# Kernel optimization log

Measured on AMD Instinct MI355X. Metric: run time of the kernel, lower is better.

The kernel has to match this reference:

```python
import jax, jax.numpy as jnp
import numpy as np

B, LQ, LK, D, H, DK = 128, 32, 128, 1024, 16, 64


def setup_inputs() -> dict:
    key = jax.random.key(0)
    ks = jax.random.split(key, 10)
    Q_seq = jax.random.normal(ks[0], (B, LQ, D), dtype=jnp.float32)
    K_seq = jax.random.normal(ks[1], (B, LK, D), dtype=jnp.float32)
    V_seq = jax.random.normal(ks[2], (B, LK, D), dtype=jnp.float32)
    title_mask = (jax.random.uniform(ks[3], (B, LQ)) < 0.9).astype(jnp.float32)
    body_mask = (jax.random.uniform(ks[4], (B, LQ, LK)) < 0.9).astype(jnp.float32)
    s = 1.0 / np.sqrt(D)
    Wq = jax.random.uniform(ks[5], (H * DK, D), jnp.float32, -s, s)
    Wk = jax.random.uniform(ks[6], (H * DK, D), jnp.float32, -s, s)
    Wv = jax.random.uniform(ks[7], (H * DK, D), jnp.float32, -s, s)
    bq = jnp.zeros((H * DK,), jnp.float32)
    bk = jnp.zeros((H * DK,), jnp.float32)
    bv = jnp.zeros((H * DK,), jnp.float32)
    return {"Q_seq": Q_seq, "K_seq": K_seq, "V_seq": V_seq,
            "title_mask": title_mask, "body_mask": body_mask,
            "Wq": Wq, "bq": bq, "Wk": Wk, "bk": bk, "Wv": Wv, "bv": bv}


def reference(Q_seq, K_seq, V_seq, title_mask, body_mask, Wq, bq, Wk, bk, Wv, bv):
    b = Q_seq.shape[0]
    # concatenate title tokens onto keys/values: [B, LK+LQ, D]
    K_cat = jnp.concatenate([K_seq, Q_seq], axis=1)
    V_cat = jnp.concatenate([V_seq, Q_seq], axis=1)
    # mask: [B, LQ, LK+LQ]
    tmask_rep = jnp.broadcast_to(title_mask[:, None, :], (b, LQ, LQ))
    mask = jnp.concatenate([body_mask, tmask_rep], axis=2) * title_mask[:, :, None]
    # projections -> [B, H, len, DK]
    Qh = (Q_seq @ Wq.T + bq).reshape(b, LQ, H, DK).transpose(0, 2, 1, 3)
    Kh = (K_cat @ Wk.T + bk).reshape(b, LK + LQ, H, DK).transpose(0, 2, 1, 3)
    Vh = (V_cat @ Wv.T + bv).reshape(b, LK + LQ, H, DK).transpose(0, 2, 1, 3)
    # custom exp-based masked attention (non-softmax normalization)
    scores = jnp.einsum('bhqd,bhkd->bhqk', Qh, Kh) / np.sqrt(float(DK))
    scores = jnp.exp(scores) * mask[:, None, :, :]
    attn = scores / (jnp.sum(scores, axis=-1, keepdims=True) + 1e-8)
    ctx = jnp.einsum('bhqk,bhkd->bhqd', attn, Vh)
    return ctx.transpose(0, 2, 1, 3).reshape(b, LQ, H * DK)
```

## Files before the change

### kernel.cpp

```cpp
#include <hip/hip_runtime.h>

typedef _Float16 f16;
typedef _Float16 f16x2 __attribute__((ext_vector_type(2)));
typedef _Float16 f16x4 __attribute__((ext_vector_type(4)));
typedef _Float16 f16x8 __attribute__((ext_vector_type(8)));
typedef float f32x4v __attribute__((ext_vector_type(4)));

#define AS1 __attribute__((address_space(1)))
#define AS3 __attribute__((address_space(3)))

__device__ __forceinline__ void gload_lds16(const f16* g, f16* l) {
  __builtin_amdgcn_global_load_lds((const AS1 unsigned int*)g,
                                   (AS3 unsigned int*)l, 16, 0, 0);
}

__global__ __launch_bounds__(256) void prep_kernel(
    const float* __restrict__ Q_seq, const float* __restrict__ K_seq,
    const float* __restrict__ V_seq,
    const float* __restrict__ Wq, const float* __restrict__ Wk,
    const float* __restrict__ Wv,
    f16* __restrict__ Qb, f16* __restrict__ Kb, f16* __restrict__ Vb,
    f16* __restrict__ Wqb, f16* __restrict__ Wkb, f16* __restrict__ Wvb)
{
  const long long g = (long long)blockIdx.x * 256 + threadIdx.x;
  const float* s;
  f16* d;
  if (g < 524288) {
    s = Q_seq + g * 8; d = Qb + g * 8;
  } else if (g < 2621440) {
    long long e = (g - 524288) * 8; s = K_seq + e; d = Kb + e;
  } else if (g < 4718592) {
    long long e = (g - 2621440) * 8; s = V_seq + e; d = Vb + e;
  } else if (g < 4849664) {
    long long e = (g - 4718592) * 8; s = Wq + e; d = Wqb + e;
  } else if (g < 4980736) {
    long long e = (g - 4849664) * 8; s = Wk + e; d = Wkb + e;
  } else {
    long long e = (g - 4980736) * 8; s = Wv + e; d = Wvb + e;
  }
  float4 v0 = *(const float4*)s;
  float4 v1 = *(const float4*)(s + 4);
  f16x8 o;
  o[0] = (f16)v0.x; o[1] = (f16)v0.y; o[2] = (f16)v0.z; o[3] = (f16)v0.w;
  o[4] = (f16)v1.x; o[5] = (f16)v1.y; o[6] = (f16)v1.z; o[7] = (f16)v1.w;
  *(f16x8*)d = o;
}

__device__ __forceinline__ void gemm_tile_256(
    const f16* __restrict__ A, const f16* __restrict__ W,
    const float* __restrict__ bias, f16* __restrict__ C,
    int m0, int n0, int rowShift, int outStride, int rowOff,
    f16* sbuf)
{
  const int t = threadIdx.x;
  const int w = t >> 6, lane = t & 63;
  const int wr = w >> 2, wc = w & 3;
  const int fr = lane & 15, g = lane >> 4;
  const int lrow = lane >> 3;
  const int kgr = (lane & 7) ^ lrow;

  const f16* aSrc[4];
  const f16* bSrc[4];
#pragma unroll
  for (int s = 0; s < 4; ++s) {
    aSrc[s] = A + (long long)(m0 + (w * 4 + s) * 8 + lrow) * 1024 + kgr * 8;
    bSrc[s] = W + (long long)(n0 + (w * 4 + s) * 8 + lrow) * 1024 + kgr * 8;
  }

#define STAGE(tile)                                                          \
  {                                                                          \
    f16* ab_ = sbuf + (((tile) & 1) << 15);                                  \
    const int ko_ = (tile) * 64;                                             \
    _Pragma("unroll") for (int s = 0; s < 4; ++s)                            \
        gload_lds16(aSrc[s] + ko_, ab_ + (w * 4 + s) * 512);                 \
    _Pragma("unroll") for (int s = 0; s < 4; ++s)                            \
        gload_lds16(bSrc[s] + ko_, ab_ + 16384 + (w * 4 + s) * 512);         \
  }

  const int gk0 = ((0 + g) ^ (fr & 7)) * 8;
  const int gk1 = ((4 + g) ^ (fr & 7)) * 8;
  const int aoff = (wr * 128 + fr) * 64;
  const int boff = (wc * 64 + fr) * 64;

  f32x4v acc[8][4];
#pragma unroll
  for (int i = 0; i < 8; ++i)
#pragma unroll
    for (int j = 0; j < 4; ++j) acc[i][j] = (f32x4v){0.f, 0.f, 0.f, 0.f};

  STAGE(0);
  STAGE(1);

  for (int tt = 0; tt < 16; ++tt) {
    if (tt < 15) {
      asm volatile("s_waitcnt vmcnt(8)" ::: "memory");
    } else {
      asm volatile("s_waitcnt vmcnt(0)" ::: "memory");
    }
    __builtin_amdgcn_s_barrier();
    __builtin_amdgcn_sched_barrier(0);

    const f16* ab = sbuf + ((tt & 1) << 15);
    const f16* bb = ab + 16384;

    f16x8 av0[8], bv0[4], av1[8], bv1[4];
#pragma unroll
    for (int i = 0; i < 8; ++i)
      av0[i] = *(const f16x8*)(ab + aoff + i * 1024 + gk0);
#pragma unroll
    for (int j = 0; j < 4; ++j)
      bv0[j] = *(const f16x8*)(bb + boff + j * 1024 + gk0);
    __builtin_amdgcn_sched_barrier(0);
#pragma unroll
    for (int i = 0; i < 8; ++i)
      av1[i] = *(const f16x8*)(ab + aoff + i * 1024 + gk1);
#pragma unroll
    for (int j = 0; j < 4; ++j)
      bv1[j] = *(const f16x8*)(bb + boff + j * 1024 + gk1);

    asm volatile("s_waitcnt lgkmcnt(12)" ::: "memory");
    __builtin_amdgcn_sched_barrier(0);
    __builtin_amdgcn_s_setprio(1);
#pragma unroll
    for (int i = 0; i < 8; ++i)
#pragma unroll
      for (int j = 0; j < 4; ++j)
        acc[i][j] = __builtin_amdgcn_mfma_f32_16x16x32_f16(av0[i], bv0[j],
                                                           acc[i][j], 0, 0, 0);
    __builtin_amdgcn_s_setprio(0);

    asm volatile("s_waitcnt lgkmcnt(0)" ::: "memory");
    __builtin_amdgcn_sched_barrier(0);
    __builtin_amdgcn_s_barrier();
    __builtin_amdgcn_sched_barrier(0);
    if (tt < 14) STAGE(tt + 2);
    __builtin_amdgcn_sched_barrier(0);
    __builtin_amdgcn_s_setprio(1);
#pragma unroll
    for (int i = 0; i < 8; ++i)
#pragma unroll
      for (int j = 0; j < 4; ++j)
        acc[i][j] = __builtin_amdgcn_mfma_f32_16x16x32_f16(av1[i], bv1[j],
                                                           acc[i][j], 0, 0, 0);
    __builtin_amdgcn_s_setprio(0);
  }
#undef STAGE

  f16* Cs = sbuf;
  float bn[4];
#pragma unroll
  for (int j = 0; j < 4; ++j) bn[j] = bias[n0 + wc * 64 + j * 16 + fr];
#pragma unroll
  for (int i = 0; i < 8; ++i) {
#pragma unroll
    for (int j = 0; j < 4; ++j) {
#pragma unroll
      for (int v = 0; v < 4; ++v) {
        int row = wr * 128 + i * 16 + g * 4 + v;
        int col = wc * 64 + j * 16 + fr;
        Cs[row * 256 + (col ^ (((row >> 2) & 7) << 3))] =
            (f16)(acc[i][j][v] + bn[j]);
      }
    }
  }
  __syncthreads();

  const int rowMask = (1 << rowShift) - 1;
  const int row = t >> 1, half = t & 1;
  const int csw = ((row >> 2) & 7) << 3;
  const int arow = m0 + row;
  const int orow = (arow >> rowShift) * outStride + (arow & rowMask) + rowOff;
  f16* dst = C + (long long)orow * 1024 + n0 + half * 128;
  const f16* srcr = Cs + row * 256;
#pragma unroll
  for (int c = 0; c < 16; ++c)
    *(f16x8*)(dst + c * 8) = *(const f16x8*)(srcr + ((half * 128 + c * 8) ^ csw));
}

__global__ __launch_bounds__(512, 1) void gemm_all(
    const f16* __restrict__ Qb, const f16* __restrict__ Kb,
    const f16* __restrict__ Vb,
    const f16* __restrict__ Wqb, const f16* __restrict__ Wkb,
    const f16* __restrict__ Wvb,
    const float* __restrict__ bq, const float* __restrict__ bk,
    const float* __restrict__ bv,
    f16* __restrict__ Qh, f16* __restrict__ Kh, f16* __restrict__ Vh)
{
  __shared__ __align__(16) f16 sbuf[65536];
  const int bid = blockIdx.x;
  const int v = (bid & 7) * 88 + (bid >> 3);

  const f16* A;
  const f16* W;
  const float* bias;
  f16* C;
  int m0, n0, rowShift, outStride, rowOff;

  if (v < 512) {
    const int z = v >> 8, rem = v & 255;
    A = z ? Vb : Kb;
    W = z ? Wvb : Wkb;
    bias = z ? bv : bk;
    C = z ? Vh : Kh;
    m0 = (rem >> 2) * 256; n0 = (rem & 3) * 256;
    rowShift = 7; outStride = 160; rowOff = 0;
  } else {
    const int u = v - 512;
    const int z = u >> 6, rem = u & 63;
    A = Qb;
    W = (z == 0) ? Wqb : (z == 1) ? Wkb : Wvb;
    bias = (z == 0) ? bq : (z == 1) ? bk : bv;
    C = (z == 0) ? Qh : (z == 1) ? Kh : Vh;
    m0 = (rem >> 2) * 256; n0 = (rem & 3) * 256;
    rowShift = 5;
    outStride = (z == 0) ? 32 : 160;
    rowOff = (z == 0) ? 0 : 128;
  }
  gemm_tile_256(A, W, bias, C, m0, n0, rowShift, outStride, rowOff, sbuf);
}

__global__ __launch_bounds__(256) void attn_kernel(
    const f16* __restrict__ Qh, const f16* __restrict__ Kh,
    const f16* __restrict__ Vh,
    const float* __restrict__ title, const float* __restrict__ body,
    float* __restrict__ out)
{
  __shared__ __align__(16) f16 Qs[32 * 72];
  __shared__ __align__(16) f16 Ks[160 * 72];
  __shared__ __align__(16) f16 Vs[160 * 68];
  __shared__ float rs[4][32];
  __shared__ float invs[32];

  const int bh = blockIdx.x, b = bh >> 4, h = bh & 15;
  const int t = threadIdx.x, w = t >> 6, lane = t & 63;
  const int c = lane & 15, g = lane >> 4;

  const long long qbase = ((long long)(b * 32) << 10) + h * 64;
  const long long kbase = ((long long)(b * 160) << 10) + h * 64;

  {
    int row = t >> 3, ch = t & 7;
    *(f16x8*)(Qs + row * 72 + ch * 8) =
        *(const f16x8*)(Qh + qbase + (long long)row * 1024 + ch * 8);
  }
#pragma unroll
  for (int r = 0; r < 5; ++r) {
    int i = t + r * 256;
    int row = i >> 3, ch = i & 7;
    *(f16x8*)(Ks + row * 72 + ch * 8) =
        *(const f16x8*)(Kh + kbase + (long long)row * 1024 + ch * 8);
    f16x8 vv = *(const f16x8*)(Vh + kbase + (long long)row * 1024 + ch * 8);
    f16x4 vlo = __builtin_shufflevector(vv, vv, 0, 1, 2, 3);
    f16x4 vhi = __builtin_shufflevector(vv, vv, 4, 5, 6, 7);
    *(f16x4*)(Vs + row * 68 + ch * 8) = vlo;
    *(f16x4*)(Vs + row * 68 + ch * 8 + 4) = vhi;
  }
  __syncthreads();

  f16x8 qf[2][2];
#pragma unroll
  for (int qt = 0; qt < 2; ++qt)
#pragma unroll
    for (int s = 0; s < 2; ++s)
      qf[qt][s] = *(const f16x8*)(Qs + (qt * 16 + c) * 72 + s * 32 + g * 8);

  const int cnt = (w < 2) ? 3 : 2;
  const int tile0 = (w < 2) ? w * 3 : 6 + (w - 2) * 2;

  f16x4 pp[3][2];
  float rsum[2] = {0.f, 0.f};

#pragma unroll
  for (int i = 0; i < 3; ++i) {
    if (i < cnt) {
      const int kt = tile0 + i;
      f16x8 kf0 = *(const f16x8*)(Ks + (kt * 16 + c) * 72 + 0 + g * 8);
      f16x8 kf1 = *(const f16x8*)(Ks + (kt * 16 + c) * 72 + 32 + g * 8);
#pragma unroll
      for (int qt = 0; qt < 2; ++qt) {
        f32x4v s4 = (f32x4v){0.f, 0.f, 0.f, 0.f};
        s4 = __builtin_amdgcn_mfma_f32_16x16x32_f16(kf0, qf[qt][0], s4, 0, 0, 0);
        s4 = __builtin_amdgcn_mfma_f32_16x16x32_f16(kf1, qf[qt][1], s4, 0, 0, 0);
        float4 m4;
        if (kt < 8) {
          m4 = *(const float4*)(body +
                ((long long)(b * 32 + qt * 16 + c)) * 128 + kt * 16 + 4 * g);
        } else {
          m4 = *(const float4*)(title + b * 32 + (kt - 8) * 16 + 4 * g);
        }
        float e0 = __expf(s4[0] * 0.125f) * m4.x;
        float e1 = __expf(s4[1] * 0.125f) * m4.y;
        float e2 = __expf(s4[2] * 0.125f) * m4.z;
        float e3 = __expf(s4[3] * 0.125f) * m4.w;
        rsum[qt] += (e0 + e1) + (e2 + e3);
        f16x4 p4;
        p4.x = (f16)e0; p4.y = (f16)e1; p4.z = (f16)e2; p4.w = (f16)e3;
        pp[i][qt] = p4;
      }
    }
  }

#pragma unroll
  for (int qt = 0; qt < 2; ++qt) {
    rsum[qt] += __shfl_xor(rsum[qt], 16);
    rsum[qt] += __shfl_xor(rsum[qt], 32);
  }
  if (lane < 16) {
    rs[w][c] = rsum[0];
    rs[w][16 + c] = rsum[1];
  }
  __syncthreads();

  f16* Ps = Ks;
#pragma unroll
  for (int i = 0; i < 3; ++i) {
    if (i < cnt) {
      const int kt = tile0 + i;
#pragma unroll
      for (int qt = 0; qt < 2; ++qt)
        *(f16x4*)(Ps + (qt * 16 + c) * 168 + kt * 16 + 4 * g) = pp[i][qt];
    }
  }
  if (t < 32) {
    float ssum = rs[0][t] + rs[1][t] + rs[2][t] + rs[3][t];
    invs[t] = title[b * 32 + t] / (ssum + 1e-8f);
  }
  __syncthreads();

  f32x4v o[2] = {(f32x4v){0.f, 0.f, 0.f, 0.f}, (f32x4v){0.f, 0.f, 0.f, 0.f}};
#pragma unroll
  for (int s = 0; s < 5; ++s) {
    f16x8 vf;
#pragma unroll
    for (int j = 0; j < 8; ++j)
      vf[j] = Vs[(32 * s + 8 * g + j) * 68 + 16 * w + c];
#pragma unroll
    for (int qt = 0; qt < 2; ++qt) {
      f16x8 pf = *(const f16x8*)(Ps + (qt * 16 + c) * 168 + s * 32 + g * 8);
      o[qt] = __builtin_amdgcn_mfma_f32_16x16x32_f16(pf, vf, o[qt], 0, 0, 0);
    }
  }

#pragma unroll
  for (int qt = 0; qt < 2; ++qt) {
#pragma unroll
    for (int v = 0; v < 4; ++v) {
      int q = qt * 16 + 4 * g + v;
      out[((long long)(b * 32 + q) << 10) + h * 64 + 16 * w + c] =
          o[qt][v] * invs[q];
    }
  }
}

extern "C" void kernel_launch(void* const* d_in, const int* in_sizes, int n_in,
                              void* d_out, int out_size, void* d_ws, size_t ws_size,
                              hipStream_t stream) {
  const float* Q_seq = (const float*)d_in[0];
  const float* K_seq = (const float*)d_in[1];
  const float* V_seq = (const float*)d_in[2];
  const float* title = (const float*)d_in[3];
  const float* body  = (const float*)d_in[4];
  const float* Wq = (const float*)d_in[5];
  const float* bq = (const float*)d_in[6];
  const float* Wk = (const float*)d_in[7];
  const float* bk = (const float*)d_in[8];
  const float* Wv = (const float*)d_in[9];
  const float* bv = (const float*)d_in[10];
  float* out = (float*)d_out;

  f16* ws = (f16*)d_ws;
  f16* Qb  = ws;
  f16* Kb  = Qb + 4194304;
  f16* Vb  = Kb + 16777216;
  f16* Wqb = Vb + 16777216;
  f16* Wkb = Wqb + 1048576;
  f16* Wvb = Wkb + 1048576;
  f16* Qh  = Wvb + 1048576;
  f16* Kh  = Qh + 4194304;
  f16* Vh  = Kh + 20971520;

  prep_kernel<<<19968, 256, 0, stream>>>(Q_seq, K_seq, V_seq, Wq, Wk, Wv,
                                         Qb, Kb, Vb, Wqb, Wkb, Wvb);
  gemm_all<<<704, 512, 0, stream>>>(Qb, Kb, Vb, Wqb, Wkb, Wvb,
                                    bq, bk, bv, Qh, Kh, Vh);
  attn_kernel<<<2048, 256, 0, stream>>>(Qh, Kh, Vh, title, body, out);
}
```

Before: 183.7 us.

## Split GEMM main loop into four barrier-synchronized LDS-read/MFMA phases

Restructures the projection GEMM inner loop from two large phases (read all 12 fragments, then 32 MFMAs) into four smaller phases. Each phase reads half the A fragments plus the B fragments and issues 16 MFMAs, with workgroup barriers between phases. The aim is to cut register pressure (fewer live f16x8 fragments) and to interleave LDS reads with MFMA work across waves in a ping-pong style. In exchange it adds many more s_barrier calls and full lgkmcnt(0) waits per iteration, which could serialize the waves.

```diff
diff --git a/kernel.cpp b/kernel.cpp
--- a/kernel.cpp
+++ b/kernel.cpp
@@ -91,59 +91,70 @@
   STAGE(0);
   STAGE(1);
 
+#define RD_A(dst, ihalf, gk)                                                 \
+  _Pragma("unroll") for (int ii = 0; ii < 4; ++ii)                           \
+      dst[ii] = *(const f16x8*)(ab + aoff + ((ihalf) * 4 + ii) * 1024 + (gk));
+#define RD_B(dst, gk)                                                        \
+  _Pragma("unroll") for (int j = 0; j < 4; ++j)                              \
+      dst[j] = *(const f16x8*)(bb + boff + j * 1024 + (gk));
+#define MFMA16(afr, bfr, ihalf)                                              \
+  __builtin_amdgcn_s_setprio(1);                                             \
+  _Pragma("unroll") for (int ii = 0; ii < 4; ++ii)                           \
+      _Pragma("unroll") for (int j = 0; j < 4; ++j)                          \
+          acc[(ihalf) * 4 + ii][j] = __builtin_amdgcn_mfma_f32_16x16x32_f16( \
+              afr[ii], bfr[j], acc[(ihalf) * 4 + ii][j], 0, 0, 0);           \
+  __builtin_amdgcn_s_setprio(0);
+
   for (int tt = 0; tt < 16; ++tt) {
     if (tt < 15) {
       asm volatile("s_waitcnt vmcnt(8)" ::: "memory");
     } else {
       asm volatile("s_waitcnt vmcnt(0)" ::: "memory");
     }
+    __builtin_amdgcn_sched_barrier(0);
     __builtin_amdgcn_s_barrier();
     __builtin_amdgcn_sched_barrier(0);
 
     const f16* ab = sbuf + ((tt & 1) << 15);
     const f16* bb = ab + 16384;
 
-    f16x8 av0[8], bv0[4], av1[8], bv1[4];
-#pragma unroll
-    for (int i = 0; i < 8; ++i)
-      av0[i] = *(const f16x8*)(ab + aoff + i * 1024 + gk0);
-#pragma unroll
-    for (int j = 0; j < 4; ++j)
-      bv0[j] = *(const f16x8*)(bb + boff + j * 1024 + gk0);
-    __builtin_amdgcn_sched_barrier(0);
-#pragma unroll
-    for (int i = 0; i < 8; ++i)
-      av1[i] = *(const f16x8*)(ab + aoff + i * 1024 + gk1);
-#pragma unroll
-    for (int j = 0; j < 4; ++j)
-      bv1[j] = *(const f16x8*)(bb + boff + j * 1024 + gk1);
-
-    asm volatile("s_waitcnt lgkmcnt(12)" ::: "memory");
-    __builtin_amdgcn_sched_barrier(0);
-    __builtin_amdgcn_s_setprio(1);
-#pragma unroll
-    for (int i = 0; i < 8; ++i)
-#pragma unroll
-      for (int j = 0; j < 4; ++j)
-        acc[i][j] = __builtin_amdgcn_mfma_f32_16x16x32_f16(av0[i], bv0[j],
-                                                           acc[i][j], 0, 0, 0);
-    __builtin_amdgcn_s_setprio(0);
-
+    f16x8 a0[4], a1[4], bf[4];
+
+    RD_A(a0, 0, gk0);
+    RD_B(bf, gk0);
+    __builtin_amdgcn_s_barrier();
     asm volatile("s_waitcnt lgkmcnt(0)" ::: "memory");
     __builtin_amdgcn_sched_barrier(0);
+    MFMA16(a0, bf, 0);
+    __builtin_amdgcn_s_barrier();
+
+    RD_A(a1, 1, gk0);
+    __builtin_amdgcn_s_barrier();
+    asm volatile("s_waitcnt lgkmcnt(0)" ::: "memory");
+    __builtin_amdgcn_sched_barrier(0);
+    MFMA16(a1, bf, 1);
+    __builtin_amdgcn_s_barrier();
+
+    RD_A(a0, 0, gk1);
+    RD_B(bf, gk1);
+    __builtin_amdgcn_s_barrier();
+    asm volatile("s_waitcnt lgkmcnt(0)" ::: "memory");
+    __builtin_amdgcn_sched_barrier(0);
+    MFMA16(a0, bf, 0);
+    __builtin_amdgcn_s_barrier();
+
+    RD_A(a1, 1, gk1);
+    asm volatile("s_waitcnt lgkmcnt(0)" ::: "memory");
+    __builtin_amdgcn_sched_barrier(0);
     __builtin_amdgcn_s_barrier();
     __builtin_amdgcn_sched_barrier(0);
     if (tt < 14) STAGE(tt + 2);
     __builtin_amdgcn_sched_barrier(0);
-    __builtin_amdgcn_s_setprio(1);
-#pragma unroll
-    for (int i = 0; i < 8; ++i)
-#pragma unroll
-      for (int j = 0; j < 4; ++j)
-        acc[i][j] = __builtin_amdgcn_mfma_f32_16x16x32_f16(av1[i], bv1[j],
-                                                           acc[i][j], 0, 0, 0);
-    __builtin_amdgcn_s_setprio(0);
-  }
+    MFMA16(a1, bf, 1);
+  }
+#undef RD_A
+#undef RD_B
+#undef MFMA16
 #undef STAGE
 
   f16* Cs = sbuf;
```

Result: slower. 189.4 us (+3.1%).

## Simplify GEMM main loop to single-stage prefetch with full barriers

Applied to the files above, without the earlier changes.

Replaces the two-deep global-to-LDS prefetch pipeline, which used hand-tuned vmcnt/lgkmcnt waits, split barriers and setprio, with a simpler scheme. Each iteration issues the next tile's loads, computes on the current buffer, and ends with __syncthreads. This removes the manual wait-count bookkeeping and priority toggling, and lets the compiler schedule the LDS reads alongside the MFMAs. In exchange, loads have only one iteration to land, and the full barrier drains all outstanding memory each step, so global latency may be less hidden.

```diff
diff --git a/kernel.cpp b/kernel.cpp
--- a/kernel.cpp
+++ b/kernel.cpp
@@ -89,60 +89,42 @@
     for (int j = 0; j < 4; ++j) acc[i][j] = (f32x4v){0.f, 0.f, 0.f, 0.f};
 
   STAGE(0);
-  STAGE(1);
+  __syncthreads();
 
   for (int tt = 0; tt < 16; ++tt) {
-    if (tt < 15) {
-      asm volatile("s_waitcnt vmcnt(8)" ::: "memory");
-    } else {
-      asm volatile("s_waitcnt vmcnt(0)" ::: "memory");
-    }
-    __builtin_amdgcn_s_barrier();
-    __builtin_amdgcn_sched_barrier(0);
-
     const f16* ab = sbuf + ((tt & 1) << 15);
     const f16* bb = ab + 16384;
 
-    f16x8 av0[8], bv0[4], av1[8], bv1[4];
+    if (tt < 15) STAGE(tt + 1);
+    __builtin_amdgcn_sched_barrier(0);
+
+    f16x8 a0[8], b0[4], a1[8], b1[4];
 #pragma unroll
     for (int i = 0; i < 8; ++i)
-      av0[i] = *(const f16x8*)(ab + aoff + i * 1024 + gk0);
+      a0[i] = *(const f16x8*)(ab + aoff + i * 1024 + gk0);
 #pragma unroll
     for (int j = 0; j < 4; ++j)
-      bv0[j] = *(const f16x8*)(bb + boff + j * 1024 + gk0);
-    __builtin_amdgcn_sched_barrier(0);
+      b0[j] = *(const f16x8*)(bb + boff + j * 1024 + gk0);
 #pragma unroll
     for (int i = 0; i < 8; ++i)
-      av1[i] = *(const f16x8*)(ab + aoff + i * 1024 + gk1);
+#pragma unroll
+      for (int j = 0; j < 4; ++j)
+        acc[i][j] = __builtin_amdgcn_mfma_f32_16x16x32_f16(a0[i], b0[j],
+                                                           acc[i][j], 0, 0, 0);
+#pragma unroll
+    for (int i = 0; i < 8; ++i)
+      a1[i] = *(const f16x8*)(ab + aoff + i * 1024 + gk1);
 #pragma unroll
     for (int j = 0; j < 4; ++j)
-      bv1[j] = *(const f16x8*)(bb + boff + j * 1024 + gk1);
-
-    asm volatile("s_waitcnt lgkmcnt(12)" ::: "memory");
-    __builtin_amdgcn_sched_barrier(0);
-    __builtin_amdgcn_s_setprio(1);
+      b1[j] = *(const f16x8*)(bb + boff + j * 1024 + gk1);
 #pragma unroll
     for (int i = 0; i < 8; ++i)
 #pragma unroll
       for (int j = 0; j < 4; ++j)
-        acc[i][j] = __builtin_amdgcn_mfma_f32_16x16x32_f16(av0[i], bv0[j],
+        acc[i][j] = __builtin_amdgcn_mfma_f32_16x16x32_f16(a1[i], b1[j],
                                                            acc[i][j], 0, 0, 0);
-    __builtin_amdgcn_s_setprio(0);
-
-    asm volatile("s_waitcnt lgkmcnt(0)" ::: "memory");
-    __builtin_amdgcn_sched_barrier(0);
-    __builtin_amdgcn_s_barrier();
-    __builtin_amdgcn_sched_barrier(0);
-    if (tt < 14) STAGE(tt + 2);
-    __builtin_amdgcn_sched_barrier(0);
-    __builtin_amdgcn_s_setprio(1);
-#pragma unroll
-    for (int i = 0; i < 8; ++i)
-#pragma unroll
-      for (int j = 0; j < 4; ++j)
-        acc[i][j] = __builtin_amdgcn_mfma_f32_16x16x32_f16(av1[i], bv1[j],
-                                                           acc[i][j], 0, 0, 0);
-    __builtin_amdgcn_s_setprio(0);
+
+    __syncthreads();
   }
 #undef STAGE
 
```

Result: no change. 182.6 us (-0.6%).

## Interleave per-unit LDS staging with quarter-split MFMA phases in projection GEMM

Applied to the files above, without the earlier changes.

Reworks the projection GEMM main loop. Global-to-LDS copies are split into eight units per tile, and the prefetch of tile tt+1 is spread across four compute sub-phases separated by barriers, instead of staging whole tiles two ahead. A fragments are now loaded per 32-row quarter rather than all at once, which cuts register pressure. The cost is a shorter prefetch distance and more workgroup barriers per k-tile.

```diff
diff --git a/kernel.cpp b/kernel.cpp
--- a/kernel.cpp
+++ b/kernel.cpp
@@ -1,7 +1,6 @@
 #include <hip/hip_runtime.h>
 
 typedef _Float16 f16;
-typedef _Float16 f16x2 __attribute__((ext_vector_type(2)));
 typedef _Float16 f16x4 __attribute__((ext_vector_type(4)));
 typedef _Float16 f16x8 __attribute__((ext_vector_type(8)));
 typedef float f32x4v __attribute__((ext_vector_type(4)));
@@ -56,30 +55,19 @@
   const int w = t >> 6, lane = t & 63;
   const int wr = w >> 2, wc = w & 3;
   const int fr = lane & 15, g = lane >> 4;
-  const int lrow = lane >> 3;
-  const int kgr = (lane & 7) ^ lrow;
-
-  const f16* aSrc[4];
-  const f16* bSrc[4];
-#pragma unroll
-  for (int s = 0; s < 4; ++s) {
-    aSrc[s] = A + (long long)(m0 + (w * 4 + s) * 8 + lrow) * 1024 + kgr * 8;
-    bSrc[s] = W + (long long)(n0 + (w * 4 + s) * 8 + lrow) * 1024 + kgr * 8;
-  }
-
-#define STAGE(tile)                                                          \
-  {                                                                          \
-    f16* ab_ = sbuf + (((tile) & 1) << 15);                                  \
-    const int ko_ = (tile) * 64;                                             \
-    _Pragma("unroll") for (int s = 0; s < 4; ++s)                            \
-        gload_lds16(aSrc[s] + ko_, ab_ + (w * 4 + s) * 512);                 \
-    _Pragma("unroll") for (int s = 0; s < 4; ++s)                            \
-        gload_lds16(bSrc[s] + ko_, ab_ + 16384 + (w * 4 + s) * 512);         \
-  }
+  const int trow = t >> 3;
+  const int kgr = (t & 7) ^ (trow & 7);
+
+  const f16* aS = A + (long long)(m0 + trow) * 1024 + kgr * 8;
+  const f16* bS = W + (long long)(n0 + trow) * 1024 + kgr * 8;
+
+#define STAGE_UNIT(u, tile)                                                  \
+  gload_lds16(((u) < 4 ? aS + ((u) * 64) * 1024 : bS + (((u) - 4) * 64) * 1024) \
+                  + (tile) * 64,                                             \
+              sbuf + (((tile) & 1) << 15) + (u) * 4096 + w * 512)
 
   const int gk0 = ((0 + g) ^ (fr & 7)) * 8;
   const int gk1 = ((4 + g) ^ (fr & 7)) * 8;
-  const int aoff = (wr * 128 + fr) * 64;
   const int boff = (wc * 64 + fr) * 64;
 
   f32x4v acc[8][4];
@@ -88,63 +76,79 @@
 #pragma unroll
     for (int j = 0; j < 4; ++j) acc[i][j] = (f32x4v){0.f, 0.f, 0.f, 0.f};
 
-  STAGE(0);
-  STAGE(1);
+#pragma unroll
+  for (int u = 0; u < 8; ++u) STAGE_UNIT(u, 0);
+  __syncthreads();
 
   for (int tt = 0; tt < 16; ++tt) {
+    const f16* ab = sbuf + ((tt & 1) << 15);
+    const f16* bb = ab + 16384;
+
+    f16x8 bv0[4], bv1[4];
+
     if (tt < 15) {
-      asm volatile("s_waitcnt vmcnt(8)" ::: "memory");
+      STAGE_UNIT(0, tt + 1); STAGE_UNIT(1, tt + 1); STAGE_UNIT(2, tt + 1);
+      asm volatile("s_waitcnt vmcnt(3)" ::: "memory");
     } else {
       asm volatile("s_waitcnt vmcnt(0)" ::: "memory");
     }
     __builtin_amdgcn_s_barrier();
-    __builtin_amdgcn_sched_barrier(0);
-
-    const f16* ab = sbuf + ((tt & 1) << 15);
-    const f16* bb = ab + 16384;
-
-    f16x8 av0[8], bv0[4], av1[8], bv1[4];
-#pragma unroll
-    for (int i = 0; i < 8; ++i)
-      av0[i] = *(const f16x8*)(ab + aoff + i * 1024 + gk0);
-#pragma unroll
-    for (int j = 0; j < 4; ++j)
-      bv0[j] = *(const f16x8*)(bb + boff + j * 1024 + gk0);
-    __builtin_amdgcn_sched_barrier(0);
-#pragma unroll
-    for (int i = 0; i < 8; ++i)
-      av1[i] = *(const f16x8*)(ab + aoff + i * 1024 + gk1);
-#pragma unroll
-    for (int j = 0; j < 4; ++j)
-      bv1[j] = *(const f16x8*)(bb + boff + j * 1024 + gk1);
-
-    asm volatile("s_waitcnt lgkmcnt(12)" ::: "memory");
-    __builtin_amdgcn_sched_barrier(0);
-    __builtin_amdgcn_s_setprio(1);
-#pragma unroll
-    for (int i = 0; i < 8; ++i)
-#pragma unroll
-      for (int j = 0; j < 4; ++j)
-        acc[i][j] = __builtin_amdgcn_mfma_f32_16x16x32_f16(av0[i], bv0[j],
-                                                           acc[i][j], 0, 0, 0);
-    __builtin_amdgcn_s_setprio(0);
-
-    asm volatile("s_waitcnt lgkmcnt(0)" ::: "memory");
-    __builtin_amdgcn_sched_barrier(0);
+
+    {
+      const int aoff = (wr * 128 + 0 * 32 + fr) * 64;
+#pragma unroll
+      for (int j = 0; j < 4; ++j) {
+        bv0[j] = *(const f16x8*)(bb + boff + j * 1024 + gk0);
+        bv1[j] = *(const f16x8*)(bb + boff + j * 1024 + gk1);
+      }
+      f16x8 a00 = *(const f16x8*)(ab + aoff + gk0);
+      f16x8 a10 = *(const f16x8*)(ab + aoff + 1024 + gk0);
+      f16x8 a01 = *(const f16x8*)(ab + aoff + gk1);
+      f16x8 a11 = *(const f16x8*)(ab + aoff + 1024 + gk1);
+      __builtin_amdgcn_s_setprio(1);
+#pragma unroll
+      for (int j = 0; j < 4; ++j) {
+        acc[0][j] = __builtin_amdgcn_mfma_f32_16x16x32_f16(a00, bv0[j], acc[0][j], 0, 0, 0);
+        acc[1][j] = __builtin_amdgcn_mfma_f32_16x16x32_f16(a10, bv0[j], acc[1][j], 0, 0, 0);
+      }
+#pragma unroll
+      for (int j = 0; j < 4; ++j) {
+        acc[0][j] = __builtin_amdgcn_mfma_f32_16x16x32_f16(a01, bv1[j], acc[0][j], 0, 0, 0);
+        acc[1][j] = __builtin_amdgcn_mfma_f32_16x16x32_f16(a11, bv1[j], acc[1][j], 0, 0, 0);
+      }
+      __builtin_amdgcn_s_setprio(0);
+    }
     __builtin_amdgcn_s_barrier();
-    __builtin_amdgcn_sched_barrier(0);
-    if (tt < 14) STAGE(tt + 2);
-    __builtin_amdgcn_sched_barrier(0);
-    __builtin_amdgcn_s_setprio(1);
-#pragma unroll
-    for (int i = 0; i < 8; ++i)
-#pragma unroll
-      for (int j = 0; j < 4; ++j)
-        acc[i][j] = __builtin_amdgcn_mfma_f32_16x16x32_f16(av1[i], bv1[j],
-                                                           acc[i][j], 0, 0, 0);
-    __builtin_amdgcn_s_setprio(0);
-  }
-#undef STAGE
+
+#pragma unroll
+    for (int q = 1; q < 4; ++q) {
+      const int aoff = (wr * 128 + q * 32 + fr) * 64;
+      f16x8 a00 = *(const f16x8*)(ab + aoff + gk0);
+      f16x8 a10 = *(const f16x8*)(ab + aoff + 1024 + gk0);
+      f16x8 a01 = *(const f16x8*)(ab + aoff + gk1);
+      f16x8 a11 = *(const f16x8*)(ab + aoff + 1024 + gk1);
+      if (tt < 15) {
+        if (q == 1) { STAGE_UNIT(3, tt + 1); STAGE_UNIT(4, tt + 1); STAGE_UNIT(5, tt + 1); }
+        if (q == 2) { STAGE_UNIT(6, tt + 1); STAGE_UNIT(7, tt + 1); }
+      }
+      __builtin_amdgcn_s_barrier();
+      __builtin_amdgcn_s_setprio(1);
+#pragma unroll
+      for (int j = 0; j < 4; ++j) {
+        acc[q * 2 + 0][j] = __builtin_amdgcn_mfma_f32_16x16x32_f16(a00, bv0[j], acc[q * 2 + 0][j], 0, 0, 0);
+        acc[q * 2 + 1][j] = __builtin_amdgcn_mfma_f32_16x16x32_f16(a10, bv0[j], acc[q * 2 + 1][j], 0, 0, 0);
+      }
+#pragma unroll
+      for (int j = 0; j < 4; ++j) {
+        acc[q * 2 + 0][j] = __builtin_amdgcn_mfma_f32_16x16x32_f16(a01, bv1[j], acc[q * 2 + 0][j], 0, 0, 0);
+        acc[q * 2 + 1][j] = __builtin_amdgcn_mfma_f32_16x16x32_f16(a11, bv1[j], acc[q * 2 + 1][j], 0, 0, 0);
+      }
+      __builtin_amdgcn_s_setprio(0);
+      __builtin_amdgcn_s_barrier();
+    }
+  }
+#undef STAGE_UNIT
+  __syncthreads();
 
   f16* Cs = sbuf;
   float bn[4];
```

Result: no change. 185.2 us (+0.8%).
